# Performance work log

Hardware: AMD Instinct MI355X
Metric: run time of the kernel (lower is better)

## Reference

```python
import jax, jax.numpy as jnp
import numpy as np

DIM, DEPTH, MULT = 512, 3, 4
E = 2 ** DEPTH            # 8 experts
HID = MULT * DIM          # 2048
B, S = 4, 1024


def setup_inputs() -> dict:
    key = jax.random.key(0)
    ks = jax.random.split(key, 7)
    sd = 1.0 / np.sqrt(DIM)
    sh = 1.0 / np.sqrt(HID)
    return {
        "x": jax.random.normal(ks[0], (B, S, DIM), dtype=jnp.float32),
        "rw": jax.random.normal(ks[1], (E - 1, DIM), dtype=jnp.float32) * sd,
        "rb": jax.random.normal(ks[2], (E - 1,), dtype=jnp.float32) * sd,
        "w1": jax.random.normal(ks[3], (E, DIM, HID), dtype=jnp.float32) * sd,
        "b1": jax.random.normal(ks[4], (E, HID), dtype=jnp.float32) * sd,
        "w2": jax.random.normal(ks[5], (E, HID, DIM), dtype=jnp.float32) * sh,
        "b2": jax.random.normal(ks[6], (E, DIM), dtype=jnp.float32) * sh,
    }


def _leaf_probs(flat_x, rw, rb):
    # Binary-tree soft routing: level d has 2**d routers at offset 2**d - 1.
    n_tok = flat_x.shape[0]
    leaf = jnp.ones((n_tok, 1), dtype=flat_x.dtype)
    for d in range(DEPTH):
        off, n = 2 ** d - 1, 2 ** d
        logits = flat_x @ rw[off:off + n].T + rb[off:off + n]   # [N, n]
        p = jax.nn.sigmoid(logits)
        # child probs: left = 1-p, right = p
        leaf = (leaf[:, :, None] * jnp.stack([1.0 - p, p], axis=2)).reshape(n_tok, 2 * n)
    return leaf  # [N, E]


def reference(x, rw, rb, w1, b1, w2, b2):
    b, s, dim = x.shape
    flat_x = x.reshape(b * s, dim)                               # [N, D]
    leaf_probs = _leaf_probs(flat_x, rw, rb)                     # [N, E]
    # Dense evaluation of all experts (soft-routing training path).
    h = jnp.einsum('nd,edh->neh', flat_x, w1) + b1[None]         # [N, E, H]
    h = jax.nn.gelu(h, approximate=False)                        # torch nn.GELU (erf)
    y = jnp.einsum('neh,ehd->ned', h, w2) + b2[None]             # [N, E, D]
    out = jnp.einsum('ned,ne->nd', y, leaf_probs)                # [N, D]
    return out.reshape(b, s, dim)
```

## Files before the change

kernel.cpp:

```cpp
#include <hip/hip_runtime.h>
#include <hip/hip_bf16.h>
#include <hip/hip_fp16.h>

#define DIM 512
#define HID 2048
#define NE 8
#define NTOK 4096

typedef _Float16 v8h __attribute__((ext_vector_type(8)));
typedef float v16f __attribute__((ext_vector_type(16)));

__device__ __forceinline__ void load16(const void* g, void* l) {
  __builtin_amdgcn_global_load_lds(
      (const __attribute__((address_space(1))) unsigned int*)g,
      (__attribute__((address_space(3))) unsigned int*)l, 16, 0, 0);
}

__device__ __forceinline__ float gelu_fast(float v) {
  float v2 = v * v;
  float u = v * __builtin_fmaf(0.07135481627f, v2, 1.5957691216f);
  float t = __expf(-u);
  return v * __builtin_amdgcn_rcpf(1.0f + t);
}

__global__ __launch_bounds__(256) void pre_kernel(const float* __restrict__ x,
                                                  const float* __restrict__ rw,
                                                  const float* __restrict__ rb,
                                                  const float* __restrict__ b2,
                                                  const float* __restrict__ w1,
                                                  const float* __restrict__ w2,
                                                  float* __restrict__ leaf,
                                                  _Float16* __restrict__ xh,
                                                  float* __restrict__ out,
                                                  _Float16* __restrict__ w1t,
                                                  _Float16* __restrict__ w2t) {
  __shared__ float tile[32][65];
  if (blockIdx.x < 1024) {
    const int lane = threadIdx.x & 63;
    const int wave = threadIdx.x >> 6;
    const int n = (blockIdx.x << 2) + wave;
    const float4* xv = (const float4*)(x + (size_t)n * DIM);
    const float4 x0 = xv[lane * 2], x1 = xv[lane * 2 + 1];
    v8h o;
    o[0] = (_Float16)x0.x; o[1] = (_Float16)x0.y; o[2] = (_Float16)x0.z; o[3] = (_Float16)x0.w;
    o[4] = (_Float16)x1.x; o[5] = (_Float16)x1.y; o[6] = (_Float16)x1.z; o[7] = (_Float16)x1.w;
    *(v8h*)(xh + (size_t)n * DIM + lane * 8) = o;
    float logits[7];
#pragma unroll
    for (int rr = 0; rr < 7; ++rr) {
      const float4* wv = (const float4*)(rw + rr * DIM);
      const float4 w0 = wv[lane * 2], w1v = wv[lane * 2 + 1];
      float s = x0.x * w0.x + x0.y * w0.y + x0.z * w0.z + x0.w * w0.w +
                x1.x * w1v.x + x1.y * w1v.y + x1.z * w1v.z + x1.w * w1v.w;
#pragma unroll
      for (int o2 = 32; o2; o2 >>= 1) s += __shfl_xor(s, o2, 64);
      logits[rr] = s + rb[rr];
    }
    const int eidx = lane & 7;
    const float p0 = 1.f / (1.f + __expf(-logits[0]));
    float f = ((eidx >> 2) & 1) ? p0 : 1.f - p0;
    const float p1 = 1.f / (1.f + __expf(-logits[1 + (eidx >> 2)]));
    f *= ((eidx >> 1) & 1) ? p1 : 1.f - p1;
    const float p2 = 1.f / (1.f + __expf(-logits[3 + (eidx >> 1)]));
    f *= (eidx & 1) ? p2 : 1.f - p2;
    if (lane < NE) leaf[(size_t)n * NE + lane] = f;
    float le[NE];
#pragma unroll
    for (int e = 0; e < NE; ++e) le[e] = __shfl(f, e, 64);
    float4 a0 = {0.f, 0.f, 0.f, 0.f}, a1 = {0.f, 0.f, 0.f, 0.f};
#pragma unroll
    for (int e = 0; e < NE; ++e) {
      const float4* bv = (const float4*)(b2 + (size_t)e * DIM + lane * 8);
      const float4 u0 = bv[0], u1 = bv[1];
      a0.x += le[e] * u0.x; a0.y += le[e] * u0.y; a0.z += le[e] * u0.z; a0.w += le[e] * u0.w;
      a1.x += le[e] * u1.x; a1.y += le[e] * u1.y; a1.z += le[e] * u1.z; a1.w += le[e] * u1.w;
    }
    float4* op = (float4*)(out + (size_t)n * DIM + lane * 8);
    op[0] = a0; op[1] = a1;
  } else {
    int bx = blockIdx.x - 1024;
    const float* in;
    _Float16* outp;
    int R, C;
    if (bx < 4096) { in = w1; outp = w1t; R = DIM; C = HID; }
    else { bx -= 4096; in = w2; outp = w2t; R = HID; C = DIM; }
    const int e = bx >> 9;
    const int rem = bx & 511;
    const int tiles_r = R >> 6;
    const int rt = rem % tiles_r;
    const int ct = rem / tiles_r;
    const int r0 = rt << 6, c0 = ct << 5;
    const size_t ebase = (size_t)e * R * C;
    const int tid = threadIdx.x;
#pragma unroll
    for (int it = 0; it < 2; ++it) {
      const int s = tid + (it << 8);
      const int row = s >> 3, cq = s & 7;
      const float4 v = *(const float4*)(in + ebase + (size_t)(r0 + row) * C + c0 + (cq << 2));
      tile[(cq << 2) + 0][row] = v.x;
      tile[(cq << 2) + 1][row] = v.y;
      tile[(cq << 2) + 2][row] = v.z;
      tile[(cq << 2) + 3][row] = v.w;
    }
    __syncthreads();
    const int c = tid >> 3, seg = tid & 7;
    v8h hv;
#pragma unroll
    for (int u = 0; u < 8; ++u) hv[u] = (_Float16)tile[c][(seg << 3) + u];
    *(v8h*)(outp + ebase + (size_t)(c0 + c) * R + r0 + (seg << 3)) = hv;
  }
}


#define WAITV6() asm volatile("s_waitcnt vmcnt(6)" ::: "memory")
#define WAITV0() asm volatile("s_waitcnt vmcnt(0)" ::: "memory")
#define BARF()                                                                \
  {                                                                           \
    __builtin_amdgcn_s_barrier();                                             \
    asm volatile("" ::: "memory");                                            \
  }

#define GEMM_STAGE(AO_LDS, BO_LDS, KOFF)                                      \
  {                                                                           \
    _Pragma("unroll") for (int p = 0; p < 4; ++p)                             \
        load16(ga[p] + (KOFF), la[p] + (AO_LDS));                             \
    _Pragma("unroll") for (int p = 0; p < 2; ++p)                             \
        load16(gb[p] + (KOFF), lb[p] + (BO_LDS));                             \
  }

#define GEMM_COMPUTE(AO, BO)                                                  \
  {                                                                           \
    v8h a[4], b[2];                                                           \
    _Pragma("unroll") for (int i = 0; i < 4; ++i)                             \
        a[i] = *(const v8h*)(fA[i] + (AO) + po0);                             \
    _Pragma("unroll") for (int j = 0; j < 2; ++j)                             \
        b[j] = *(const v8h*)(fB[j] + (BO) + po0);                             \
    __builtin_amdgcn_s_setprio(1);                                            \
    _Pragma("unroll") for (int i = 0; i < 4; ++i)                             \
        _Pragma("unroll") for (int j = 0; j < 2; ++j)                         \
            acc[i][j] = __builtin_amdgcn_mfma_f32_32x32x16_f16(a[i], b[j], acc[i][j], 0, 0, 0); \
    __builtin_amdgcn_s_setprio(0);                                            \
    _Pragma("unroll") for (int i = 0; i < 4; ++i)                             \
        a[i] = *(const v8h*)(fA[i] + (AO) + (po0 ^ 16));                      \
    _Pragma("unroll") for (int j = 0; j < 2; ++j)                             \
        b[j] = *(const v8h*)(fB[j] + (BO) + (po0 ^ 16));                      \
    __builtin_amdgcn_s_setprio(1);                                            \
    _Pragma("unroll") for (int i = 0; i < 4; ++i)                             \
        _Pragma("unroll") for (int j = 0; j < 2; ++j)                         \
            acc[i][j] = __builtin_amdgcn_mfma_f32_32x32x16_f16(a[i], b[j], acc[i][j], 0, 0, 0); \
    __builtin_amdgcn_s_setprio(0);                                            \
  }

#define GEMM_PIPE_ITER()                                                      \
  {                                                                           \
    WAITV6(); BARF();                                                         \
    GEMM_COMPUTE(0, 0);                                                       \
    BARF();                                                                   \
    GEMM_STAGE(0, 0, 64);                                                     \
    WAITV6(); BARF();                                                         \
    GEMM_COMPUTE(8192, 4096);                                                 \
    BARF();                                                                   \
    GEMM_STAGE(8192, 4096, 96);                                               \
    _Pragma("unroll") for (int p = 0; p < 4; ++p) ga[p] += 64;                \
    _Pragma("unroll") for (int p = 0; p < 2; ++p) gb[p] += 64;                \
  }

#define GEMM_PIPE_TAIL()                                                      \
  {                                                                           \
    WAITV6(); BARF();                                                         \
    GEMM_COMPUTE(0, 0);                                                       \
    WAITV0(); BARF();                                                         \
    GEMM_COMPUTE(8192, 4096);                                                 \
  }

__global__ __launch_bounds__(256, 2) void gemm1_kernel(const _Float16* __restrict__ xh,
                                                       const _Float16* __restrict__ w1t,
                                                       const float* __restrict__ b1,
                                                       const float* __restrict__ leaf,
                                                       _Float16* __restrict__ H) {
  const int bx = blockIdx.x;
  const int e = bx & 7;
  const int t = bx >> 3;
  const int mt = t & 15;
  const int nt = t >> 4;
  const int m0 = mt << 8, n0 = nt << 7;

  __shared__ alignas(16) _Float16 As[2 * 256 * 32];
  __shared__ alignas(16) _Float16 Bs[2 * 128 * 32];

  const int tid = threadIdx.x;
  const int lane = tid & 63;
  const int wave = tid >> 6;
  const int wm = wave >> 1, wn = wave & 1;
  const int c = lane & 31, h2 = lane >> 5;
  const int swz = (c >> 1) & 3;
  const int po0 = (h2 ^ swz) << 3;

  const _Float16* ga[4];
  const _Float16* gb[2];
  _Float16* la[4];
  _Float16* lb[2];
#pragma unroll
  for (int p = 0; p < 4; ++p) {
    const int ci = (p << 8) + tid;
    const int row = ci >> 2;
    const int lg = (ci & 3) ^ ((row >> 1) & 3);
    ga[p] = xh + (size_t)(m0 + row) * DIM + (lg << 3);
    la[p] = As + (ci << 3);
  }
#pragma unroll
  for (int p = 0; p < 2; ++p) {
    const int ci = (p << 8) + tid;
    const int row = ci >> 2;
    const int lg = (ci & 3) ^ ((row >> 1) & 3);
    gb[p] = w1t + ((size_t)e * HID + n0 + row) * DIM + (lg << 3);
    lb[p] = Bs + (ci << 3);
  }
  const _Float16* fA[4];
  const _Float16* fB[2];
#pragma unroll
  for (int i = 0; i < 4; ++i) fA[i] = As + (((wm << 7) + (i << 5) + c) << 5);
#pragma unroll
  for (int j = 0; j < 2; ++j) fB[j] = Bs + (((wn << 6) + (j << 5) + c) << 5);

  v16f acc[4][2];
#pragma unroll
  for (int i = 0; i < 4; ++i)
#pragma unroll
    for (int j = 0; j < 2; ++j)
      acc[i][j] = v16f{0.f,0.f,0.f,0.f,0.f,0.f,0.f,0.f,0.f,0.f,0.f,0.f,0.f,0.f,0.f,0.f};

  GEMM_STAGE(0, 0, 0);
  GEMM_STAGE(8192, 4096, 32);
  for (int gp = 0; gp < 7; ++gp) GEMM_PIPE_ITER();
  GEMM_PIPE_TAIL();

  const float* b1e = b1 + (size_t)e * HID;
  _Float16* He = H + (size_t)e * NTOK * HID;
  const int colb = n0 + (wn << 6) + c;
  const float bias0 = b1e[colb];
  const float bias1 = b1e[colb + 32];
#pragma unroll
  for (int i = 0; i < 4; ++i) {
    const int rb0 = m0 + (wm << 7) + (i << 5) + (h2 << 2);
#pragma unroll
    for (int rg = 0; rg < 4; ++rg) {
#pragma unroll
      for (int rr = 0; rr < 4; ++rr) {
        const int row = rb0 + (rg << 3) + rr;
        const int reg = (rg << 2) + rr;
        const float p = leaf[(size_t)row * NE + e];
        _Float16* hp = He + (size_t)row * HID + colb;
        hp[0]  = (_Float16)(p * gelu_fast(acc[i][0][reg] + bias0));
        hp[32] = (_Float16)(p * gelu_fast(acc[i][1][reg] + bias1));
      }
    }
  }
}

__global__ __launch_bounds__(256, 2) void gemm2_kernel(const _Float16* __restrict__ H,
                                                       const _Float16* __restrict__ w2t,
                                                       float* __restrict__ out) {
  const int bx = blockIdx.x;
  const int e = bx & 7;
  const int dt = (bx >> 3) & 3;
  const int mt = bx >> 5;
  const int m0 = mt << 8, d0 = dt << 7;

  __shared__ alignas(16) _Float16 As[2 * 256 * 32];
  __shared__ alignas(16) _Float16 Bs[2 * 128 * 32];

  const int tid = threadIdx.x;
  const int lane = tid & 63;
  const int wave = tid >> 6;
  const int wm = wave >> 1, wn = wave & 1;
  const int c = lane & 31, h2 = lane >> 5;
  const int swz = (c >> 1) & 3;
  const int po0 = (h2 ^ swz) << 3;

  const _Float16* ga[4];
  const _Float16* gb[2];
  _Float16* la[4];
  _Float16* lb[2];
#pragma unroll
  for (int p = 0; p < 4; ++p) {
    const int ci = (p << 8) + tid;
    const int row = ci >> 2;
    const int lg = (ci & 3) ^ ((row >> 1) & 3);
    ga[p] = H + ((size_t)e * NTOK + m0 + row) * HID + (lg << 3);
    la[p] = As + (ci << 3);
  }
#pragma unroll
  for (int p = 0; p < 2; ++p) {
    const int ci = (p << 8) + tid;
    const int row = ci >> 2;
    const int lg = (ci & 3) ^ ((row >> 1) & 3);
    gb[p] = w2t + ((size_t)e * DIM + d0 + row) * HID + (lg << 3);
    lb[p] = Bs + (ci << 3);
  }
  const _Float16* fA[4];
  const _Float16* fB[2];
#pragma unroll
  for (int i = 0; i < 4; ++i) fA[i] = As + (((wm << 7) + (i << 5) + c) << 5);
#pragma unroll
  for (int j = 0; j < 2; ++j) fB[j] = Bs + (((wn << 6) + (j << 5) + c) << 5);

  v16f acc[4][2];
#pragma unroll
  for (int i = 0; i < 4; ++i)
#pragma unroll
    for (int j = 0; j < 2; ++j)
      acc[i][j] = v16f{0.f,0.f,0.f,0.f,0.f,0.f,0.f,0.f,0.f,0.f,0.f,0.f,0.f,0.f,0.f,0.f};

  GEMM_STAGE(0, 0, 0);
  GEMM_STAGE(8192, 4096, 32);
  for (int gp = 0; gp < 31; ++gp) GEMM_PIPE_ITER();
  GEMM_PIPE_TAIL();

#pragma unroll
  for (int i = 0; i < 4; ++i) {
    const int rb0 = m0 + (wm << 7) + (i << 5) + (h2 << 2);
#pragma unroll
    for (int rg = 0; rg < 4; ++rg) {
#pragma unroll
      for (int rr = 0; rr < 4; ++rr) {
        const int row = rb0 + (rg << 3) + rr;
        const int reg = (rg << 2) + rr;
        float* op = out + (size_t)row * DIM + d0 + (wn << 6) + c;
        atomicAdd(op, acc[i][0][reg]);
        atomicAdd(op + 32, acc[i][1][reg]);
      }
    }
  }
}

extern "C" void kernel_launch(void* const* d_in, const int* in_sizes, int n_in,
                              void* d_out, int out_size, void* d_ws, size_t ws_size,
                              hipStream_t stream) {
  const float* x  = (const float*)d_in[0];
  const float* rw = (const float*)d_in[1];
  const float* rb = (const float*)d_in[2];
  const float* w1 = (const float*)d_in[3];
  const float* b1 = (const float*)d_in[4];
  const float* w2 = (const float*)d_in[5];
  const float* b2 = (const float*)d_in[6];
  float* out = (float*)d_out;

  char* ws = (char*)d_ws;
  const size_t xh_bytes   = (size_t)NTOK * DIM * 2;
  const size_t w1t_bytes  = (size_t)NE * HID * DIM * 2;
  const size_t w2t_bytes  = (size_t)NE * DIM * HID * 2;
  const size_t leaf_bytes = (size_t)NTOK * NE * 4;
  const size_t H_bytes    = (size_t)NE * NTOK * HID * 2;
  _Float16* xh   = (_Float16*)(ws);
  _Float16* w1t  = (_Float16*)(ws + xh_bytes);
  _Float16* w2t  = (_Float16*)(ws + xh_bytes + w1t_bytes);
  float*    leaf = (float*)(ws + xh_bytes + w1t_bytes + w2t_bytes);
  _Float16* Hbuf = (_Float16*)(ws + xh_bytes + w1t_bytes + w2t_bytes + leaf_bytes);
  if (ws_size < xh_bytes + w1t_bytes + w2t_bytes + leaf_bytes + H_bytes) return;

  pre_kernel<<<9216, 256, 0, stream>>>(x, rw, rb, b2, w1, w2, leaf, xh, out, w1t, w2t);
  gemm1_kernel<<<2048, 256, 0, stream>>>(xh, w1t, b1, leaf, Hbuf);
  gemm2_kernel<<<512, 256, 0, stream>>>(Hbuf, w2t, out);
}
```

Measured before the change: 350.4 us.

## Triple-buffer A tiles with staggered B prefetch in both expert GEMMs

```diff
diff --git a/kernel.cpp b/kernel.cpp
--- a/kernel.cpp
+++ b/kernel.cpp
@@ -112,18 +112,22 @@
 }
 
 
-#define WAITV6() asm volatile("s_waitcnt vmcnt(6)" ::: "memory")
-#define WAITV0() asm volatile("s_waitcnt vmcnt(0)" ::: "memory")
+#define WAIT10() asm volatile("s_waitcnt vmcnt(10)" ::: "memory")
+#define WAIT6()  asm volatile("s_waitcnt vmcnt(6)" ::: "memory")
+#define WAIT0()  asm volatile("s_waitcnt vmcnt(0)" ::: "memory")
 #define BARF()                                                                \
   {                                                                           \
     __builtin_amdgcn_s_barrier();                                             \
     asm volatile("" ::: "memory");                                            \
   }
 
-#define GEMM_STAGE(AO_LDS, BO_LDS, KOFF)                                      \
+#define STAGE_A(AO_LDS, KOFF)                                                 \
   {                                                                           \
     _Pragma("unroll") for (int p = 0; p < 4; ++p)                             \
         load16(ga[p] + (KOFF), la[p] + (AO_LDS));                             \
+  }
+#define STAGE_B(BO_LDS, KOFF)                                                 \
+  {                                                                           \
     _Pragma("unroll") for (int p = 0; p < 2; ++p)                             \
         load16(gb[p] + (KOFF), lb[p] + (BO_LDS));                             \
   }
@@ -151,26 +155,47 @@
     __builtin_amdgcn_s_setprio(0);                                            \
   }
 
-#define GEMM_PIPE_ITER()                                                      \
-  {                                                                           \
-    WAITV6(); BARF();                                                         \
-    GEMM_COMPUTE(0, 0);                                                       \
+#define FULL_ITER(a3, b2, kA, kB)                                             \
+  {                                                                           \
+    WAIT10(); BARF();                                                         \
+    GEMM_COMPUTE((a3) * 8192, (b2) * 4096);                                   \
     BARF();                                                                   \
-    GEMM_STAGE(0, 0, 64);                                                     \
-    WAITV6(); BARF();                                                         \
+    STAGE_B((b2) * 4096, (kB));                                               \
+    STAGE_A((a3) * 8192, (kA));                                               \
+  }
+
+#define ITER6()                                                               \
+  {                                                                           \
+    FULL_ITER(0, 0, 96, 64);                                                  \
+    FULL_ITER(1, 1, 128, 96);                                                 \
+    FULL_ITER(2, 0, 160, 128);                                                \
+    FULL_ITER(0, 1, 192, 160);                                                \
+    FULL_ITER(1, 0, 224, 192);                                                \
+    FULL_ITER(2, 1, 256, 224);                                                \
+    _Pragma("unroll") for (int p = 0; p < 4; ++p) ga[p] += 192;               \
+    _Pragma("unroll") for (int p = 0; p < 2; ++p) gb[p] += 192;               \
+  }
+
+#define TAIL4()                                                               \
+  {                                                                           \
+    FULL_ITER(0, 0, 96, 64);                                                  \
+    WAIT10(); BARF();                                                         \
     GEMM_COMPUTE(8192, 4096);                                                 \
     BARF();                                                                   \
-    GEMM_STAGE(8192, 4096, 96);                                               \
-    _Pragma("unroll") for (int p = 0; p < 4; ++p) ga[p] += 64;                \
-    _Pragma("unroll") for (int p = 0; p < 2; ++p) gb[p] += 64;                \
-  }
-
-#define GEMM_PIPE_TAIL()                                                      \
-  {                                                                           \
-    WAITV6(); BARF();                                                         \
-    GEMM_COMPUTE(0, 0);                                                       \
-    WAITV0(); BARF();                                                         \
-    GEMM_COMPUTE(8192, 4096);                                                 \
+    STAGE_B(4096, 96);                                                        \
+    WAIT6(); BARF();                                                          \
+    GEMM_COMPUTE(16384, 0);                                                   \
+    WAIT0(); BARF();                                                          \
+    GEMM_COMPUTE(0, 4096);                                                    \
+  }
+
+#define PROLOGUE()                                                            \
+  {                                                                           \
+    STAGE_A(0, 0);                                                            \
+    STAGE_B(0, 0);                                                            \
+    STAGE_A(8192, 32);                                                        \
+    STAGE_B(4096, 32);                                                        \
+    STAGE_A(16384, 64);                                                       \
   }
 
 __global__ __launch_bounds__(256, 2) void gemm1_kernel(const _Float16* __restrict__ xh,
@@ -185,7 +210,7 @@
   const int nt = t >> 4;
   const int m0 = mt << 8, n0 = nt << 7;
 
-  __shared__ alignas(16) _Float16 As[2 * 256 * 32];
+  __shared__ alignas(16) _Float16 As[3 * 256 * 32];
   __shared__ alignas(16) _Float16 Bs[2 * 128 * 32];
 
   const int tid = threadIdx.x;
@@ -230,10 +255,9 @@
     for (int j = 0; j < 2; ++j)
       acc[i][j] = v16f{0.f,0.f,0.f,0.f,0.f,0.f,0.f,0.f,0.f,0.f,0.f,0.f,0.f,0.f,0.f,0.f};
 
-  GEMM_STAGE(0, 0, 0);
-  GEMM_STAGE(8192, 4096, 32);
-  for (int gp = 0; gp < 7; ++gp) GEMM_PIPE_ITER();
-  GEMM_PIPE_TAIL();
+  PROLOGUE();
+  for (int s = 0; s < 2; ++s) ITER6();
+  TAIL4();
 
   const float* b1e = b1 + (size_t)e * HID;
   _Float16* He = H + (size_t)e * NTOK * HID;
@@ -267,7 +291,7 @@
   const int mt = bx >> 5;
   const int m0 = mt << 8, d0 = dt << 7;
 
-  __shared__ alignas(16) _Float16 As[2 * 256 * 32];
+  __shared__ alignas(16) _Float16 As[3 * 256 * 32];
   __shared__ alignas(16) _Float16 Bs[2 * 128 * 32];
 
   const int tid = threadIdx.x;
@@ -312,10 +336,9 @@
     for (int j = 0; j < 2; ++j)
       acc[i][j] = v16f{0.f,0.f,0.f,0.f,0.f,0.f,0.f,0.f,0.f,0.f,0.f,0.f,0.f,0.f,0.f,0.f};
 
-  GEMM_STAGE(0, 0, 0);
-  GEMM_STAGE(8192, 4096, 32);
-  for (int gp = 0; gp < 31; ++gp) GEMM_PIPE_ITER();
-  GEMM_PIPE_TAIL();
+  PROLOGUE();
+  for (int s = 0; s < 10; ++s) ITER6();
+  TAIL4();
 
 #pragma unroll
   for (int i = 0; i < 4; ++i) {
```

Measured after the change: 349.8 us. About the same (-0.2%).
